# Optimization experiments

Measured on AMD Instinct MI355X. Metric: run time of the kernel, lower is better.

## Reference

```python
import jax, jax.numpy as jnp
import numpy as np

N_FILTERS = 10
# torch.linspace(2,100,10).to(int32) truncates toward zero
CELL_SIZES = np.linspace(2, 100, N_FILTERS).astype(np.int32)  # [2,12,23,34,45,56,67,78,89,100]
B, N = 16384, 4096


def setup_inputs() -> dict:
    key = jax.random.key(0)
    k1, k2, k3 = jax.random.split(key, 3)
    inp = jax.random.normal(k1, (B, N), dtype=jnp.float32)
    # DoA search grid in radians
    search_space = jax.random.uniform(k2, (N,), dtype=jnp.float32,
                                      minval=-jnp.pi / 2, maxval=jnp.pi / 2)
    w = jax.random.normal(k3, (1, N_FILTERS), dtype=jnp.float32) / 100 + 1.0 / N_FILTERS
    b = jnp.zeros((1,), dtype=jnp.float32)
    return {"inp": inp, "search_space": search_space, "w": w, "b": b}


def _top_peak(x):
    # vectorized replacement for the per-batch scipy.signal.find_peaks + sort:
    # a peak is a strict local max; pick the peak with the largest spectrum value.
    interior = (x[:, 1:-1] > x[:, :-2]) & (x[:, 1:-1] > x[:, 2:])  # [B, N-2]
    mask = jnp.pad(interior, ((0, 0), (1, 1)))                      # [B, N]
    scores = jnp.where(mask, x, -jnp.inf)
    return jnp.argmax(scores, axis=1)  # [B] int


def reference(inp, search_space, w, b):
    n = inp.shape[1]
    top1 = _top_peak(inp)  # [B], non-differentiable index
    outs = []
    for c in CELL_SIZES:
        c = int(c)
        offs = jnp.arange(-c, c)                       # [2c]
        idx = (top1[:, None] + offs[None, :]) % n      # [B, 2c] circular window
        vals = jnp.take_along_axis(inp, idx, axis=1)   # [B, 2c]
        sm = jax.nn.softmax(vals, axis=1)
        outs.append(jnp.sum(search_space[idx] * sm, axis=1))  # [B]
    feat = jnp.stack(outs, axis=1)                     # [B, 10]
    return jax.nn.relu(feat @ w.T + b)                 # [B, 1]
```

## Files before the change

kernel.cpp:

```cpp
#include <hip/hip_runtime.h>
#include <math.h>

#define N_COLS 4096
#define WIN 200
#define CENTER 100

__global__ __launch_bounds__(256, 4) void filter_kernel(
    const float* __restrict__ inp,
    const float* __restrict__ ss,
    const float* __restrict__ wt,
    const float* __restrict__ bias,
    float* __restrict__ out,
    int B)
{
    const int wave = threadIdx.x >> 6;
    const int lane = threadIdx.x & 63;
    const int row  = blockIdx.x;
    if (row >= B) return;

    const float* __restrict__ x = inp + (size_t)row * N_COLS;

    __shared__ float s_bestv[4];
    __shared__ int   s_besti[4];
    __shared__ float s_acc[4];

    const int base = wave * 1024;
    float4 v[4];
    #pragma unroll
    for (int c = 0; c < 4; ++c)
        v[c] = *reinterpret_cast<const float4*>(x + base + c * 256 + lane * 4);

    float seamL = 0.0f, seamR = 0.0f;
    if (lane == 0  && base > 0)               seamL = x[base - 1];
    if (lane == 63 && base + 1024 < N_COLS)   seamR = x[base + 1024];

    float bestv = -INFINITY;
    int   besti = 0;

    #pragma unroll
    for (int c = 0; c < 4; ++c) {
        const int p = base + c * 256 + lane * 4;
        const float4 cc = v[c];

        float left  = __shfl_up(cc.w, 1, 64);
        float right = __shfl_down(cc.x, 1, 64);
        if (c > 0) { const float e0 = __shfl(v[c - 1].w, 63, 64); if (lane == 0)  left  = e0; }
        else       { if (lane == 0)  left  = seamL; }
        if (c < 3) { const float e1 = __shfl(v[c + 1].x, 0, 64);  if (lane == 63) right = e1; }
        else       { if (lane == 63) right = seamR; }

        if (p >= 1 && cc.x > left && cc.x > cc.y && cc.x > bestv) { bestv = cc.x; besti = p; }
        if (cc.y > cc.x && cc.y > cc.z && cc.y > bestv)           { bestv = cc.y; besti = p + 1; }
        if (cc.z > cc.y && cc.z > cc.w && cc.z > bestv)           { bestv = cc.z; besti = p + 2; }
        if (p + 3 <= N_COLS - 2 && cc.w > cc.z && cc.w > right && cc.w > bestv) {
            bestv = cc.w; besti = p + 3;
        }
    }

    #pragma unroll
    for (int off = 32; off >= 1; off >>= 1) {
        float ov = __shfl_xor(bestv, off, 64);
        int   oi = __shfl_xor(besti, off, 64);
        if (ov > bestv || (ov == bestv && oi < besti)) { bestv = ov; besti = oi; }
    }
    if (lane == 0) { s_bestv[wave] = bestv; s_besti[wave] = besti; }
    __syncthreads();

    float bv = s_bestv[0]; int bi = s_besti[0];
    #pragma unroll
    for (int k = 1; k < 4; ++k) {
        const float ov = s_bestv[k]; const int oi = s_besti[k];
        if (ov > bv || (ov == bv && oi < bi)) { bv = ov; bi = oi; }
    }
    const int top1 = bi;

    float e[4], t[4];
    #pragma unroll
    for (int q = 0; q < 4; ++q) {
        const int j = lane + q * 64;
        const int pos = (top1 - CENTER + j) & (N_COLS - 1);
        const float xv = x[pos];
        const float sv = ss[pos];
        e[q] = (j < WIN) ? __expf(xv) : 0.0f;
        t[q] = e[q] * sv;
    }

    float accw = 0.0f;
    #pragma unroll
    for (int i = 0; i < 3; ++i) {
        const int f = wave + i * 4;
        if (f < 10) {
            const int cell = (18 + 98 * f) / 9;
            const int lo = CENTER - cell;
            const int hi = CENTER + cell;
            float s1 = 0.0f, s2 = 0.0f;
            #pragma unroll
            for (int q = 0; q < 4; ++q) {
                const int j = lane + q * 64;
                if (j >= lo && j < hi) { s1 += e[q]; s2 += t[q]; }
            }
            #pragma unroll
            for (int off = 32; off >= 1; off >>= 1) {
                s1 += __shfl_xor(s1, off, 64);
                s2 += __shfl_xor(s2, off, 64);
            }
            accw += (s2 / s1) * wt[f];
        }
    }
    if (lane == 0) s_acc[wave] = accw;
    __syncthreads();

    if (threadIdx.x == 0) {
        const float r = s_acc[0] + s_acc[1] + s_acc[2] + s_acc[3] + bias[0];
        out[row] = r > 0.0f ? r : 0.0f;
    }
}

extern "C" void kernel_launch(void* const* d_in, const int* in_sizes, int n_in,
                              void* d_out, int out_size, void* d_ws, size_t ws_size,
                              hipStream_t stream) {
    const float* inp  = (const float*)d_in[0];
    const float* ss   = (const float*)d_in[1];
    const float* wt   = (const float*)d_in[2];
    const float* bias = (const float*)d_in[3];
    float* out = (float*)d_out;

    const int B = in_sizes[0] / N_COLS;
    filter_kernel<<<B, 256, 0, stream>>>(inp, ss, wt, bias, out, B);
}
```

Baseline: 357.6 us.

## Split fused kernel into peak-finding and window-reduction kernels

Breaks the single per-row kernel into two. The first kernel finds the top peak for two rows per block and writes the indices to workspace. The second kernel computes the windowed softmax features with one wave per row. This frees the bandwidth-bound scan from the latency-bound gather and reduction tail and removes a block barrier there. In exchange it adds a second launch and a workspace round trip, and the window gathers may miss cache because the row is no longer resident.

```diff
diff --git a/kernel.cpp b/kernel.cpp
--- a/kernel.cpp
+++ b/kernel.cpp
@@ -5,38 +5,11 @@
 #define WIN 200
 #define CENTER 100
 
-__global__ __launch_bounds__(256, 4) void filter_kernel(
-    const float* __restrict__ inp,
-    const float* __restrict__ ss,
-    const float* __restrict__ wt,
-    const float* __restrict__ bias,
-    float* __restrict__ out,
-    int B)
+__device__ __forceinline__ void scan_quarter(
+    const float4* __restrict__ v, int base, int lane, float seamL, float seamR,
+    float& bestv, int& besti)
 {
-    const int wave = threadIdx.x >> 6;
-    const int lane = threadIdx.x & 63;
-    const int row  = blockIdx.x;
-    if (row >= B) return;
-
-    const float* __restrict__ x = inp + (size_t)row * N_COLS;
-
-    __shared__ float s_bestv[4];
-    __shared__ int   s_besti[4];
-    __shared__ float s_acc[4];
-
-    const int base = wave * 1024;
-    float4 v[4];
-    #pragma unroll
-    for (int c = 0; c < 4; ++c)
-        v[c] = *reinterpret_cast<const float4*>(x + base + c * 256 + lane * 4);
-
-    float seamL = 0.0f, seamR = 0.0f;
-    if (lane == 0  && base > 0)               seamL = x[base - 1];
-    if (lane == 63 && base + 1024 < N_COLS)   seamR = x[base + 1024];
-
-    float bestv = -INFINITY;
-    int   besti = 0;
-
+    bestv = -INFINITY; besti = 0;
     #pragma unroll
     for (int c = 0; c < 4; ++c) {
         const int p = base + c * 256 + lane * 4;
@@ -56,62 +29,117 @@
             bestv = cc.w; besti = p + 3;
         }
     }
-
     #pragma unroll
     for (int off = 32; off >= 1; off >>= 1) {
-        float ov = __shfl_xor(bestv, off, 64);
-        int   oi = __shfl_xor(besti, off, 64);
+        const float ov = __shfl_xor(bestv, off, 64);
+        const int   oi = __shfl_xor(besti, off, 64);
         if (ov > bestv || (ov == bestv && oi < besti)) { bestv = ov; besti = oi; }
     }
-    if (lane == 0) { s_bestv[wave] = bestv; s_besti[wave] = besti; }
+}
+
+__global__ __launch_bounds__(256) void peak_kernel(
+    const float* __restrict__ inp,
+    int* __restrict__ top1,
+    int B)
+{
+    const int wave = threadIdx.x >> 6;
+    const int lane = threadIdx.x & 63;
+    const int r0   = blockIdx.x * 2;
+    if (r0 >= B) return;
+
+    const float* __restrict__ xA = inp + (size_t)r0 * N_COLS;
+    const float* __restrict__ xB = xA + N_COLS;
+
+    __shared__ float s_bv[2][4];
+    __shared__ int   s_bi[2][4];
+
+    const int base = wave * 1024;
+
+    float4 va[4], vb[4];
+    #pragma unroll
+    for (int c = 0; c < 4; ++c)
+        va[c] = *reinterpret_cast<const float4*>(xA + base + c * 256 + lane * 4);
+    #pragma unroll
+    for (int c = 0; c < 4; ++c)
+        vb[c] = *reinterpret_cast<const float4*>(xB + base + c * 256 + lane * 4);
+
+    float seamLA = 0.f, seamRA = 0.f, seamLB = 0.f, seamRB = 0.f;
+    if (lane == 0 && base > 0) {
+        seamLA = xA[base - 1]; seamLB = xB[base - 1];
+    }
+    if (lane == 63 && base + 1024 < N_COLS) {
+        seamRA = xA[base + 1024]; seamRB = xB[base + 1024];
+    }
+
+    float bv; int bi;
+    scan_quarter(va, base, lane, seamLA, seamRA, bv, bi);
+    if (lane == 0) { s_bv[0][wave] = bv; s_bi[0][wave] = bi; }
+    scan_quarter(vb, base, lane, seamLB, seamRB, bv, bi);
+    if (lane == 0) { s_bv[1][wave] = bv; s_bi[1][wave] = bi; }
     __syncthreads();
 
-    float bv = s_bestv[0]; int bi = s_besti[0];
-    #pragma unroll
-    for (int k = 1; k < 4; ++k) {
-        const float ov = s_bestv[k]; const int oi = s_besti[k];
-        if (ov > bv || (ov == bv && oi < bi)) { bv = ov; bi = oi; }
+    if (threadIdx.x == 0 || threadIdx.x == 64) {
+        const int r = threadIdx.x >> 6;
+        float v0 = s_bv[r][0]; int i0 = s_bi[r][0];
+        #pragma unroll
+        for (int k = 1; k < 4; ++k) {
+            const float ov = s_bv[r][k]; const int oi = s_bi[r][k];
+            if (ov > v0 || (ov == v0 && oi < i0)) { v0 = ov; i0 = oi; }
+        }
+        top1[r0 + r] = i0;
     }
-    const int top1 = bi;
+}
+
+__global__ __launch_bounds__(256) void window_kernel(
+    const float* __restrict__ inp,
+    const float* __restrict__ ss,
+    const float* __restrict__ wt,
+    const float* __restrict__ bias,
+    const int* __restrict__ top1,
+    float* __restrict__ out,
+    int B)
+{
+    const int wave = threadIdx.x >> 6;
+    const int lane = threadIdx.x & 63;
+    const int row  = blockIdx.x * 4 + wave;
+    if (row >= B) return;
+
+    const float* __restrict__ x = inp + (size_t)row * N_COLS;
+    const int t1 = top1[row];
 
     float e[4], t[4];
     #pragma unroll
     for (int q = 0; q < 4; ++q) {
         const int j = lane + q * 64;
-        const int pos = (top1 - CENTER + j) & (N_COLS - 1);
+        const int pos = (t1 - CENTER + j) & (N_COLS - 1);
         const float xv = x[pos];
         const float sv = ss[pos];
         e[q] = (j < WIN) ? __expf(xv) : 0.0f;
         t[q] = e[q] * sv;
     }
 
-    float accw = 0.0f;
+    const int cells[10] = {2, 12, 23, 34, 45, 56, 67, 78, 89, 100};
+    float acc = 0.0f;
     #pragma unroll
-    for (int i = 0; i < 3; ++i) {
-        const int f = wave + i * 4;
-        if (f < 10) {
-            const int cell = (18 + 98 * f) / 9;
-            const int lo = CENTER - cell;
-            const int hi = CENTER + cell;
-            float s1 = 0.0f, s2 = 0.0f;
-            #pragma unroll
-            for (int q = 0; q < 4; ++q) {
-                const int j = lane + q * 64;
-                if (j >= lo && j < hi) { s1 += e[q]; s2 += t[q]; }
-            }
-            #pragma unroll
-            for (int off = 32; off >= 1; off >>= 1) {
-                s1 += __shfl_xor(s1, off, 64);
-                s2 += __shfl_xor(s2, off, 64);
-            }
-            accw += (s2 / s1) * wt[f];
+    for (int f = 0; f < 10; ++f) {
+        const int lo = CENTER - cells[f];
+        const int hi = CENTER + cells[f];
+        float s1 = 0.0f, s2 = 0.0f;
+        #pragma unroll
+        for (int q = 0; q < 4; ++q) {
+            const int j = lane + q * 64;
+            if (j >= lo && j < hi) { s1 += e[q]; s2 += t[q]; }
         }
+        #pragma unroll
+        for (int off = 32; off >= 1; off >>= 1) {
+            s1 += __shfl_xor(s1, off, 64);
+            s2 += __shfl_xor(s2, off, 64);
+        }
+        acc += (s2 / s1) * wt[f];
     }
-    if (lane == 0) s_acc[wave] = accw;
-    __syncthreads();
 
-    if (threadIdx.x == 0) {
-        const float r = s_acc[0] + s_acc[1] + s_acc[2] + s_acc[3] + bias[0];
+    if (lane == 0) {
+        const float r = acc + bias[0];
         out[row] = r > 0.0f ? r : 0.0f;
     }
 }
@@ -124,7 +152,9 @@
     const float* wt   = (const float*)d_in[2];
     const float* bias = (const float*)d_in[3];
     float* out = (float*)d_out;
+    int* top1 = (int*)d_ws;
 
     const int B = in_sizes[0] / N_COLS;
-    filter_kernel<<<B, 256, 0, stream>>>(inp, ss, wt, bias, out, B);
+    peak_kernel<<<(B + 1) / 2, 256, 0, stream>>>(inp, top1, B);
+    window_kernel<<<(B + 3) / 4, 256, 0, stream>>>(inp, ss, wt, bias, top1, out, B);
 }
```

After: 383.7 us. 7.3% more time.
